# Optimization experiments

Hardware: AMD Instinct MI355X
Metric: run time of the kernel (lower is better)

Reference implementation:

```python
import jax, jax.numpy as jnp
import numpy as np

B, S, D, H = 256, 512, 200, 256

def setup_inputs() -> dict:
    key = jax.random.key(0)
    ks = jax.random.split(key, 10)
    scale = 1.0 / np.sqrt(D + H)
    all_input = jax.random.normal(ks[0], (B, S, D), dtype=jnp.float32)
    # realistic variable-length mask: first L tokens valid per example
    lengths = jax.random.randint(ks[1], (B,), S // 4, S + 1)
    mask = (jnp.arange(S)[None, :] < lengths[:, None]).astype(jnp.float32)
    def W(k):
        return jax.random.normal(k, (D + H, H), dtype=jnp.float32) * scale
    return {
        "all_input": all_input,
        "mask": mask,
        "Wi": W(ks[2]), "bi": jnp.zeros((H,), jnp.float32),
        "Wf": W(ks[3]), "bf": jnp.zeros((H,), jnp.float32),
        "Wo": W(ks[4]), "bo": jnp.zeros((H,), jnp.float32),
        "Wz": W(ks[5]), "bz": jnp.zeros((H,), jnp.float32),
    }

def reference(all_input, mask, Wi, bi, Wf, bf, Wo, bo, Wz, bz):
    # manually unrolled LSTM (4 gate Linears over concat(x, h)), zero init state
    def step(carry, xt):
        h, c = carry
        xh = jnp.concatenate([xt, h], axis=1)          # [B, D+H]
        i = jax.nn.sigmoid(xh @ Wi + bi)
        f = jax.nn.sigmoid(xh @ Wf + bf)
        o = jax.nn.sigmoid(xh @ Wo + bo)
        z = jnp.tanh(xh @ Wz + bz)
        c_new = i * z + f * c
        h_new = o * jnp.tanh(c_new)
        return (h_new, c_new), h_new

    h0 = jnp.zeros((all_input.shape[0], Wi.shape[1]), all_input.dtype)
    c0 = jnp.zeros_like(h0)
    xs = jnp.swapaxes(all_input, 0, 1)                  # [S, B, D]
    _, h_all = jax.lax.scan(step, (h0, c0), xs)         # [S, B, H]
    h_all = jnp.swapaxes(h_all, 0, 1)                   # [B, S, H]
    masked_h = h_all * mask[:, :, None]
    # return_average=True: masked mean over time
    return jnp.sum(masked_h, axis=1) / jnp.sum(mask, axis=1, keepdims=True)
```

## Files before the change

kernel.cpp:

```cpp
#include <hip/hip_runtime.h>
#include <hip/hip_fp16.h>

#define B_ 256
#define S_ 512
#define D_ 200
#define H_ 256

typedef _Float16 half2_t __attribute__((ext_vector_type(2)));
typedef _Float16 half4_t __attribute__((ext_vector_type(4)));
typedef _Float16 half8_t __attribute__((ext_vector_type(8)));
typedef float    floatx4 __attribute__((ext_vector_type(4)));

__device__ __forceinline__ float fast_sig(float x) {
    return 1.f / (1.f + __expf(-x));
}
__device__ __forceinline__ float fast_tanh(float x) {
    x = fminf(15.f, fmaxf(-15.f, x));
    float e = __expf(2.f * x);
    return (e - 1.f) / (e + 1.f);
}

__global__ void prep(const float* __restrict__ Wi, const float* __restrict__ Wf,
                     const float* __restrict__ Wo, const float* __restrict__ Wz,
                     _Float16* __restrict__ W4T, _Float16* __restrict__ WhT) {
    const int n = blockIdx.x;
    const int t = threadIdx.x;
    const int g = n >> 8, j = n & 255;
    const float* Wg = (g == 0) ? Wi : (g == 1) ? Wf : (g == 2) ? Wo : Wz;
    if (t < 224)
        W4T[(size_t)n * 224 + t] = (t < D_) ? (_Float16)Wg[t * 256 + j] : (_Float16)0.f;
    WhT[(size_t)n * 256 + t] = (_Float16)Wg[(D_ + t) * 256 + j];
}

__global__ __launch_bounds__(256) void gemm_x(const float* __restrict__ X,
                                              const _Float16* __restrict__ W4T,
                                              const float* __restrict__ bi,
                                              const float* __restrict__ bfg,
                                              const float* __restrict__ bo,
                                              const float* __restrict__ bz,
                                              _Float16* __restrict__ G) {
    __shared__ __align__(16) _Float16 As[128][40];
    __shared__ __align__(16) _Float16 Bs[128][40];

    const int mt = blockIdx.x >> 3;
    const int nt = blockIdx.x & 7;
    const int m0 = mt * 128, n0 = nt * 128;
    const int tid  = threadIdx.x;
    const int lane = tid & 63, wave = tid >> 6;
    const int quad = lane >> 4, l16 = lane & 15;
    const int mq = (wave & 1) * 64, nq = (wave >> 1) * 64;

    floatx4 acc[4][4];
#pragma unroll
    for (int i = 0; i < 4; ++i)
#pragma unroll
        for (int j = 0; j < 4; ++j) acc[i][j] = (floatx4){0.f, 0.f, 0.f, 0.f};

    const int srow = tid >> 1;
    const int koff = (tid & 1) * 16;

    for (int kt = 0; kt < 7; ++kt) {
        const int k0 = kt * 32;
        {
            const int m = m0 + srow;
            const float* xr = X + (size_t)m * D_ + (k0 + koff);
            half8_t v0, v1;
            if (m < B_ * S_ - 1) {
                const floatx4* xp = (const floatx4*)xr;
                floatx4 f0 = xp[0], f1 = xp[1], f2 = xp[2], f3 = xp[3];
#pragma unroll
                for (int i = 0; i < 4; ++i) {
                    v0[i]     = (_Float16)f0[i];
                    v0[4 + i] = (_Float16)f1[i];
                    v1[i]     = (_Float16)f2[i];
                    v1[4 + i] = (_Float16)f3[i];
                }
            } else {
#pragma unroll
                for (int i = 0; i < 8; ++i) {
                    int k = k0 + koff + i;
                    v0[i] = (k < D_) ? (_Float16)xr[i] : (_Float16)0.f;
                }
#pragma unroll
                for (int i = 0; i < 8; ++i) {
                    int k = k0 + koff + 8 + i;
                    v1[i] = (k < D_) ? (_Float16)xr[8 + i] : (_Float16)0.f;
                }
            }
            *(half8_t*)&As[srow][koff]     = v0;
            *(half8_t*)&As[srow][koff + 8] = v1;
        }
        {
            const _Float16* wr = W4T + (size_t)(n0 + srow) * 224 + (k0 + koff);
            const half8_t* wp = (const half8_t*)wr;
            *(half8_t*)&Bs[srow][koff]     = wp[0];
            *(half8_t*)&Bs[srow][koff + 8] = wp[1];
        }
        __syncthreads();

        half8_t af[4], bf[4];
#pragma unroll
        for (int i = 0; i < 4; ++i) af[i] = *(const half8_t*)&As[mq + i * 16 + l16][quad * 8];
#pragma unroll
        for (int i = 0; i < 4; ++i) bf[i] = *(const half8_t*)&Bs[nq + i * 16 + l16][quad * 8];
#pragma unroll
        for (int mi = 0; mi < 4; ++mi)
#pragma unroll
            for (int ni = 0; ni < 4; ++ni)
                acc[mi][ni] = __builtin_amdgcn_mfma_f32_16x16x32_f16(af[mi], bf[ni], acc[mi][ni], 0, 0, 0);
        __syncthreads();
    }

#pragma unroll
    for (int ni = 0; ni < 4; ++ni) {
        const int gcol = n0 + nq + ni * 16 + l16;
        const int g = gcol >> 8, j = gcol & 255;
        const float bv = ((g == 0) ? bi : (g == 1) ? bfg : (g == 2) ? bo : bz)[j];
#pragma unroll
        for (int mi = 0; mi < 4; ++mi)
#pragma unroll
            for (int r = 0; r < 4; ++r) {
                const int grow = m0 + mq + mi * 16 + quad * 4 + r;
                G[(size_t)grow * 1024 + gcol] = (_Float16)(acc[mi][ni][r] + bv);
            }
    }
}

__global__ __launch_bounds__(512, 2) void lstm_rec(
    const _Float16* __restrict__ G,
    const _Float16* __restrict__ WhT,
    const float* __restrict__ mask,
    float* __restrict__ out)
{
    __shared__ __align__(16) half8_t  WLfrag[8192];
    __shared__ __align__(16) _Float16 hS[2][256];

    const int b    = blockIdx.x;
    const int t    = threadIdx.x;
    const int w    = t >> 6;
    const int lane = t & 63;
    const int l16  = lane & 15, quad = lane >> 4;

#pragma unroll
    for (int mi = 0; mi < 8; ++mi) {
        const int gcol = ((mi & 3) << 8) + (2 * w + (mi >> 2)) * 16 + l16;
        const half8_t* src = (const half8_t*)(WhT + (size_t)gcol * 256);
        WLfrag[((w * 8 + mi) * 2 + 0) * 64 + lane] = src[6 * 4 + quad];
        WLfrag[((w * 8 + mi) * 2 + 1) * 64 + lane] = src[7 * 4 + quad];
    }

#define DECLF(mi) half8_t F##mi##_0, F##mi##_1, F##mi##_2, F##mi##_3, F##mi##_4, F##mi##_5
#define LOADF(mi) do {                                                        \
        const int gcol = ((mi & 3) << 8) + (2 * w + ((mi) >> 2)) * 16 + l16;  \
        const half8_t* p = (const half8_t*)(WhT + (size_t)gcol * 256);        \
        F##mi##_0 = p[0 * 4 + quad]; F##mi##_1 = p[1 * 4 + quad];             \
        F##mi##_2 = p[2 * 4 + quad]; F##mi##_3 = p[3 * 4 + quad];             \
        F##mi##_4 = p[4 * 4 + quad]; F##mi##_5 = p[5 * 4 + quad];             \
        asm volatile("" : "+v"(F##mi##_0), "+v"(F##mi##_1), "+v"(F##mi##_2),  \
                          "+v"(F##mi##_3), "+v"(F##mi##_4), "+v"(F##mi##_5)); \
    } while (0)
    DECLF(0); DECLF(1); DECLF(2); DECLF(3); DECLF(4); DECLF(5); DECLF(6); DECLF(7);
    LOADF(0); LOADF(1); LOADF(2); LOADF(3); LOADF(4); LOADF(5); LOADF(6); LOADF(7);

    if (t < 256) hS[0][t] = (_Float16)0.f;

    const int jbh_c = (l16 >> 2) & 1;
    const int r_c   = l16 & 3;
    const int j     = 32 * w + jbh_c * 16 + quad * 4 + r_c;

    float cst = 0.f, accum = 0.f, msum = 0.f;
    const float* mb = mask + (size_t)b * S_;

    const _Float16* Gbase = G + ((size_t)b << 19) + 32 * w + quad * 4;

    half4_t N0, N1, N2, N3, N4, N5, N6, N7;
#define GLOAD(sidx) do {                                                      \
        const _Float16* gp = Gbase + ((size_t)(sidx) << 10);                  \
        N0 = *(const half4_t*)(gp + 0);   N1 = *(const half4_t*)(gp + 256);   \
        N2 = *(const half4_t*)(gp + 512); N3 = *(const half4_t*)(gp + 768);   \
        N4 = *(const half4_t*)(gp + 16);  N5 = *(const half4_t*)(gp + 272);   \
        N6 = *(const half4_t*)(gp + 528); N7 = *(const half4_t*)(gp + 784);   \
    } while (0)

    GLOAD(0);
    __syncthreads();

#define MFALL(kt, Bv)                                                          \
    C0 = __builtin_amdgcn_mfma_f32_16x16x32_f16(F0_##kt, Bv, C0, 0, 0, 0);     \
    C1 = __builtin_amdgcn_mfma_f32_16x16x32_f16(F1_##kt, Bv, C1, 0, 0, 0);     \
    C2 = __builtin_amdgcn_mfma_f32_16x16x32_f16(F2_##kt, Bv, C2, 0, 0, 0);     \
    C3 = __builtin_amdgcn_mfma_f32_16x16x32_f16(F3_##kt, Bv, C3, 0, 0, 0);     \
    C4 = __builtin_amdgcn_mfma_f32_16x16x32_f16(F4_##kt, Bv, C4, 0, 0, 0);     \
    C5 = __builtin_amdgcn_mfma_f32_16x16x32_f16(F5_##kt, Bv, C5, 0, 0, 0);     \
    C6 = __builtin_amdgcn_mfma_f32_16x16x32_f16(F6_##kt, Bv, C6, 0, 0, 0);     \
    C7 = __builtin_amdgcn_mfma_f32_16x16x32_f16(F7_##kt, Bv, C7, 0, 0, 0)

#define MFLDS(ktL, Bv)                                                         \
    C0 = __builtin_amdgcn_mfma_f32_16x16x32_f16(WLfrag[((w*8+0)*2+(ktL))*64+lane], Bv, C0, 0, 0, 0); \
    C1 = __builtin_amdgcn_mfma_f32_16x16x32_f16(WLfrag[((w*8+1)*2+(ktL))*64+lane], Bv, C1, 0, 0, 0); \
    C2 = __builtin_amdgcn_mfma_f32_16x16x32_f16(WLfrag[((w*8+2)*2+(ktL))*64+lane], Bv, C2, 0, 0, 0); \
    C3 = __builtin_amdgcn_mfma_f32_16x16x32_f16(WLfrag[((w*8+3)*2+(ktL))*64+lane], Bv, C3, 0, 0, 0); \
    C4 = __builtin_amdgcn_mfma_f32_16x16x32_f16(WLfrag[((w*8+4)*2+(ktL))*64+lane], Bv, C4, 0, 0, 0); \
    C5 = __builtin_amdgcn_mfma_f32_16x16x32_f16(WLfrag[((w*8+5)*2+(ktL))*64+lane], Bv, C5, 0, 0, 0); \
    C6 = __builtin_amdgcn_mfma_f32_16x16x32_f16(WLfrag[((w*8+6)*2+(ktL))*64+lane], Bv, C6, 0, 0, 0); \
    C7 = __builtin_amdgcn_mfma_f32_16x16x32_f16(WLfrag[((w*8+7)*2+(ktL))*64+lane], Bv, C7, 0, 0, 0)

    for (int s = 0; s < S_; ++s) {
        const float m = mb[s];
        const _Float16* hb = hS[s & 1];

        half8_t Bv0 = *(const half8_t*)(hb + 0 * 32 + quad * 8);
        half8_t Bv1 = *(const half8_t*)(hb + 1 * 32 + quad * 8);
        half8_t Bv2 = *(const half8_t*)(hb + 2 * 32 + quad * 8);
        half8_t Bv3 = *(const half8_t*)(hb + 3 * 32 + quad * 8);

        floatx4 C0, C1, C2, C3, C4, C5, C6, C7;
#pragma unroll
        for (int k = 0; k < 4; ++k) {
            C0[k] = (float)N0[k]; C1[k] = (float)N1[k];
            C2[k] = (float)N2[k]; C3[k] = (float)N3[k];
            C4[k] = (float)N4[k]; C5[k] = (float)N5[k];
            C6[k] = (float)N6[k]; C7[k] = (float)N7[k];
        }
        GLOAD((s < S_ - 1) ? s + 1 : s);

        MFALL(0, Bv0);
        half8_t Bv4 = *(const half8_t*)(hb + 4 * 32 + quad * 8);
        half8_t Bv5 = *(const half8_t*)(hb + 5 * 32 + quad * 8);
        MFALL(1, Bv1);
        half8_t Bv6 = *(const half8_t*)(hb + 6 * 32 + quad * 8);
        half8_t Bv7 = *(const half8_t*)(hb + 7 * 32 + quad * 8);
        MFALL(2, Bv2);
        MFALL(3, Bv3);
        MFLDS(0, Bv6);
        MFLDS(1, Bv7);
        MFALL(4, Bv4);
        MFALL(5, Bv5);

        floatx4 s0 = jbh_c ? C4 : C0;
        floatx4 s1 = jbh_c ? C5 : C1;
        floatx4 s2 = jbh_c ? C6 : C2;
        floatx4 s3 = jbh_c ? C7 : C3;
        float pre0, pre1, pre2, pre3;
        {
            float v01 = (r_c & 1) ? s0[1] : s0[0], v23 = (r_c & 1) ? s0[3] : s0[2];
            pre0 = (r_c & 2) ? v23 : v01;
            v01 = (r_c & 1) ? s1[1] : s1[0]; v23 = (r_c & 1) ? s1[3] : s1[2];
            pre1 = (r_c & 2) ? v23 : v01;
            v01 = (r_c & 1) ? s2[1] : s2[0]; v23 = (r_c & 1) ? s2[3] : s2[2];
            pre2 = (r_c & 2) ? v23 : v01;
            v01 = (r_c & 1) ? s3[1] : s3[0]; v23 = (r_c & 1) ? s3[3] : s3[2];
            pre3 = (r_c & 2) ? v23 : v01;
        }
        const float fi = fast_sig(pre0);
        const float ff = fast_sig(pre1);
        const float fo = fast_sig(pre2);
        const float fz = fast_tanh(pre3);
        cst = fi * fz + ff * cst;
        const float h = fo * fast_tanh(cst);
        accum += m * h;
        msum  += m;
        if (l16 < 8) hS[(s + 1) & 1][j] = (_Float16)h;
        __syncthreads();
    }
#undef MFALL
#undef MFLDS
#undef DECLF
#undef LOADF
#undef GLOAD

    if (l16 < 8) out[b * 256 + j] = accum / msum;
}

extern "C" void kernel_launch(void* const* d_in, const int* in_sizes, int n_in,
                              void* d_out, int out_size, void* d_ws, size_t ws_size,
                              hipStream_t stream) {
    const float* X    = (const float*)d_in[0];
    const float* mask = (const float*)d_in[1];
    const float* Wi   = (const float*)d_in[2];
    const float* bi   = (const float*)d_in[3];
    const float* Wf   = (const float*)d_in[4];
    const float* bf   = (const float*)d_in[5];
    const float* Wo   = (const float*)d_in[6];
    const float* bo   = (const float*)d_in[7];
    const float* Wz   = (const float*)d_in[8];
    const float* bz   = (const float*)d_in[9];
    float* out = (float*)d_out;

    char* ws = (char*)d_ws;
    _Float16* G   = (_Float16*)ws;
    _Float16* W4T = (_Float16*)(ws + (size_t)B_ * S_ * 1024 * 2);
    _Float16* WhT = (_Float16*)(ws + (size_t)B_ * S_ * 1024 * 2 + (size_t)1024 * 224 * 2);

    hipLaunchKernelGGL(prep,     dim3(1024), dim3(256), 0, stream, Wi, Wf, Wo, Wz, W4T, WhT);
    hipLaunchKernelGGL(gemm_x,   dim3(8192), dim3(256), 0, stream, X, W4T, bi, bf, bo, bz, G);
    hipLaunchKernelGGL(lstm_rec, dim3(B_),   dim3(512), 0, stream, G, WhT, mask, out);
}
```

Before: 1.302 ms.

## Replace per-step block barrier with per-wave flag dataflow sync in LSTM recurrence

Removes the __syncthreads at the end of each time step. Instead, each wave publishes its finished hidden-state slice through a workgroup-scope flag in shared memory. Consumers spin on each chunk's flag before loading that slice and running its MFMAs, and each wave starts from a different chunk in rotated order. The aim is to let waves overlap their recurrent matmul with slower waves' activation work instead of all stalling at a full barrier. The cost is spin-wait traffic on LDS, a larger per-wave code path, and correctness that now depends on memory ordering and on the flags being initialised before any wave stores to them.

```diff
diff --git a/kernel.cpp b/kernel.cpp
--- a/kernel.cpp
+++ b/kernel.cpp
@@ -126,7 +126,7 @@
     }
 }
 
-__global__ __launch_bounds__(512, 2) void lstm_rec(
+__global__ __launch_bounds__(512, 2) void lstm_rec9(
     const _Float16* __restrict__ G,
     const _Float16* __restrict__ WhT,
     const float* __restrict__ mask,
@@ -134,6 +134,7 @@
 {
     __shared__ __align__(16) half8_t  WLfrag[8192];
     __shared__ __align__(16) _Float16 hS[2][256];
+    __shared__ int flagS[8];
 
     const int b    = blockIdx.x;
     const int t    = threadIdx.x;
@@ -163,6 +164,7 @@
     LOADF(0); LOADF(1); LOADF(2); LOADF(3); LOADF(4); LOADF(5); LOADF(6); LOADF(7);
 
     if (t < 256) hS[0][t] = (_Float16)0.f;
+    if (t < 8)   flagS[t] = 0;
 
     const int jbh_c = (l16 >> 2) & 1;
     const int r_c   = l16 & 3;
@@ -205,14 +207,30 @@
     C6 = __builtin_amdgcn_mfma_f32_16x16x32_f16(WLfrag[((w*8+6)*2+(ktL))*64+lane], Bv, C6, 0, 0, 0); \
     C7 = __builtin_amdgcn_mfma_f32_16x16x32_f16(WLfrag[((w*8+7)*2+(ktL))*64+lane], Bv, C7, 0, 0, 0)
 
+#define DO0(Bv) MFALL(0, Bv)
+#define DO1(Bv) MFALL(1, Bv)
+#define DO2(Bv) MFALL(2, Bv)
+#define DO3(Bv) MFALL(3, Bv)
+#define DO4(Bv) MFALL(4, Bv)
+#define DO5(Bv) MFALL(5, Bv)
+#define DO6(Bv) MFLDS(0, Bv)
+#define DO7(Bv) MFLDS(1, Bv)
+
+#define CHUNK(c) do {                                                          \
+        while (__hip_atomic_load(&flagS[c], __ATOMIC_RELAXED,                  \
+                                 __HIP_MEMORY_SCOPE_WORKGROUP) < s) {}         \
+        asm volatile("" ::: "memory");                                         \
+        half8_t Bv = *(const half8_t*)(hb + (c) * 32 + quad * 8);              \
+        DO##c(Bv);                                                             \
+    } while (0)
+
+#define SEQ(c0, c1, c2, c3, c4, c5, c6, c7)                                    \
+    CHUNK(c0); CHUNK(c1); CHUNK(c2); CHUNK(c3);                                \
+    CHUNK(c4); CHUNK(c5); CHUNK(c6); CHUNK(c7)
+
     for (int s = 0; s < S_; ++s) {
         const float m = mb[s];
         const _Float16* hb = hS[s & 1];
-
-        half8_t Bv0 = *(const half8_t*)(hb + 0 * 32 + quad * 8);
-        half8_t Bv1 = *(const half8_t*)(hb + 1 * 32 + quad * 8);
-        half8_t Bv2 = *(const half8_t*)(hb + 2 * 32 + quad * 8);
-        half8_t Bv3 = *(const half8_t*)(hb + 3 * 32 + quad * 8);
 
         floatx4 C0, C1, C2, C3, C4, C5, C6, C7;
 #pragma unroll
@@ -224,18 +242,16 @@
         }
         GLOAD((s < S_ - 1) ? s + 1 : s);
 
-        MFALL(0, Bv0);
-        half8_t Bv4 = *(const half8_t*)(hb + 4 * 32 + quad * 8);
-        half8_t Bv5 = *(const half8_t*)(hb + 5 * 32 + quad * 8);
-        MFALL(1, Bv1);
-        half8_t Bv6 = *(const half8_t*)(hb + 6 * 32 + quad * 8);
-        half8_t Bv7 = *(const half8_t*)(hb + 7 * 32 + quad * 8);
-        MFALL(2, Bv2);
-        MFALL(3, Bv3);
-        MFLDS(0, Bv6);
-        MFLDS(1, Bv7);
-        MFALL(4, Bv4);
-        MFALL(5, Bv5);
+        switch (w) {
+            case 0: SEQ(0, 1, 2, 3, 4, 5, 6, 7); break;
+            case 1: SEQ(1, 2, 3, 4, 5, 6, 7, 0); break;
+            case 2: SEQ(2, 3, 4, 5, 6, 7, 0, 1); break;
+            case 3: SEQ(3, 4, 5, 6, 7, 0, 1, 2); break;
+            case 4: SEQ(4, 5, 6, 7, 0, 1, 2, 3); break;
+            case 5: SEQ(5, 6, 7, 0, 1, 2, 3, 4); break;
+            case 6: SEQ(6, 7, 0, 1, 2, 3, 4, 5); break;
+            default: SEQ(7, 0, 1, 2, 3, 4, 5, 6); break;
+        }
 
         floatx4 s0 = jbh_c ? C4 : C0;
         floatx4 s1 = jbh_c ? C5 : C1;
@@ -260,11 +276,25 @@
         const float h = fo * fast_tanh(cst);
         accum += m * h;
         msum  += m;
+
         if (l16 < 8) hS[(s + 1) & 1][j] = (_Float16)h;
-        __syncthreads();
+        asm volatile("s_waitcnt lgkmcnt(0)" ::: "memory");
+        if (lane == 0)
+            __hip_atomic_store(&flagS[w], s + 1, __ATOMIC_RELAXED,
+                               __HIP_MEMORY_SCOPE_WORKGROUP);
     }
 #undef MFALL
 #undef MFLDS
+#undef DO0
+#undef DO1
+#undef DO2
+#undef DO3
+#undef DO4
+#undef DO5
+#undef DO6
+#undef DO7
+#undef CHUNK
+#undef SEQ
 #undef DECLF
 #undef LOADF
 #undef GLOAD
@@ -292,7 +322,7 @@
     _Float16* W4T = (_Float16*)(ws + (size_t)B_ * S_ * 1024 * 2);
     _Float16* WhT = (_Float16*)(ws + (size_t)B_ * S_ * 1024 * 2 + (size_t)1024 * 224 * 2);
 
-    hipLaunchKernelGGL(prep,     dim3(1024), dim3(256), 0, stream, Wi, Wf, Wo, Wz, W4T, WhT);
-    hipLaunchKernelGGL(gemm_x,   dim3(8192), dim3(256), 0, stream, X, W4T, bi, bf, bo, bz, G);
-    hipLaunchKernelGGL(lstm_rec, dim3(B_),   dim3(512), 0, stream, G, WhT, mask, out);
-}
+    hipLaunchKernelGGL(prep,      dim3(1024), dim3(256), 0, stream, Wi, Wf, Wo, Wz, W4T, WhT);
+    hipLaunchKernelGGL(gemm_x,    dim3(8192), dim3(256), 0, stream, X, W4T, bi, bf, bo, bz, G);
+    hipLaunchKernelGGL(lstm_rec9, dim3(B_),   dim3(512), 0, stream, G, WhT, mask, out);
+}
```

New measurement: 4.286 ms. 3.29x slower.
